# Performance work log

Measured on AMD Instinct MI355X. Metric: run time of the kernel, lower is better.

## Reference

```python
import jax, jax.numpy as jnp
import numpy as np

N = 50000      # nodes per type
E = 200000     # edges per relation
H, D = 4, 64   # heads, per-head dim
C = H * D      # hidden = hc_graph * heads = 256
L = 3          # num_hops (HGTConv layers)
HC_LIN, HC_TASK = 256, 128
OUT_DIMS = (3, 3, 3, 5, 1, 1, 8)  # ptr_l1/l2/l3, leaf_category, signed, floating, size


def setup_inputs() -> dict:
    key = jax.random.key(0)
    ks = jax.random.split(key, 24)
    f = lambda k, s: jax.random.normal(k, s, dtype=jnp.float32) * 0.05
    ri = lambda k: jax.random.randint(k, (E,), 0, N, dtype=jnp.int32)
    return {
        "xe": f(ks[0], (N, C)),
        "xs": f(ks[1], (N, C)),
        "ee_src": ri(ks[2]), "ee_dst": ri(ks[3]),
        "es_src": ri(ks[4]), "es_dst": ri(ks[5]),
        "se_src": ri(ks[6]), "se_dst": ri(ks[7]),
        # per-layer, per-node-type projections (2 node types)
        "Wk": f(ks[8], (L, 2, C, C)),
        "Wq": f(ks[9], (L, 2, C, C)),
        "Wv": f(ks[10], (L, 2, C, C)),
        "Wa": f(ks[11], (L, 2, C, C)),
        "skip": jnp.ones((L, 2), dtype=jnp.float32),
        # per-layer, per-relation attention/message transforms (3 relations)
        "Arel": f(ks[12], (L, 3, H, D, D)),
        "Mrel": f(ks[13], (L, 3, H, D, D)),
        "mu": jnp.ones((L, 3, H), dtype=jnp.float32),
        # shared linear stack + 7 task heads (final out padded to 8, sliced per head)
        "Wsh": f(ks[14], (2, HC_LIN, HC_LIN)),
        "bsh": jnp.zeros((2, HC_LIN), dtype=jnp.float32),
        "Wt1": f(ks[15], (7, HC_LIN, HC_TASK)),
        "bt1": jnp.zeros((7, HC_TASK), dtype=jnp.float32),
        "Wt2": f(ks[16], (7, HC_TASK, 8)),
        "bt2": jnp.zeros((7, 8), dtype=jnp.float32),
    }


def _seg_softmax(scores, seg, n):
    m = jax.ops.segment_max(scores, seg, num_segments=n)
    e = jnp.exp(scores - m[seg])
    s = jax.ops.segment_sum(e, seg, num_segments=n)
    return e / (s[seg] + 1e-16)


def _hgt_forward(xe, xs, ee_src, ee_dst, es_src, es_dst, se_src, se_dst,
                 Wk, Wq, Wv, Wa, skip, Arel, Mrel, mu, Wsh, bsh, Wt1, bt1, Wt2, bt2):
    inv_sqrt_d = 1.0 / jnp.sqrt(jnp.float32(D))

    def rel(k_src, v_src, q_dst, src, dst, A, M, m):
        kt = jnp.einsum('ehd,hdf->ehf', k_src[src], A)          # [E,H,D]
        score = (q_dst[dst] * kt).sum(-1) * (m * inv_sqrt_d)    # [E,H]
        msg = jnp.einsum('ehd,hdf->ehf', v_src[src], M)         # [E,H,D]
        return score, msg

    for l in range(L):
        ke = (xe @ Wk[l, 0]).reshape(N, H, D)
        qe = (xe @ Wq[l, 0]).reshape(N, H, D)
        ve = (xe @ Wv[l, 0]).reshape(N, H, D)
        ks_ = (xs @ Wk[l, 1]).reshape(N, H, D)
        qs = (xs @ Wq[l, 1]).reshape(N, H, D)
        vs = (xs @ Wv[l, 1]).reshape(N, H, D)

        s0, m0 = rel(ke, ve, qe, ee_src, ee_dst, Arel[l, 0], Mrel[l, 0], mu[l, 0])  # expr->expr
        s1, m1 = rel(ke, ve, qs, es_src, es_dst, Arel[l, 1], Mrel[l, 1], mu[l, 1])  # expr->stmt
        s2, m2 = rel(ks_, vs, qe, se_src, se_dst, Arel[l, 2], Mrel[l, 2], mu[l, 2])  # stmt->expr

        # destination 'expr': softmax over all incoming edges (rel0 + rel2)
        sc_e = jnp.concatenate([s0, s2], axis=0)
        ms_e = jnp.concatenate([m0, m2], axis=0)
        dst_e = jnp.concatenate([ee_dst, se_dst], axis=0)
        a_e = _seg_softmax(sc_e, dst_e, N)
        agg_e = jax.ops.segment_sum(a_e[..., None] * ms_e, dst_e, num_segments=N).reshape(N, C)

        # destination 'stmt': only rel1
        a_s = _seg_softmax(s1, es_dst, N)
        agg_s = jax.ops.segment_sum(a_s[..., None] * m1, es_dst, num_segments=N).reshape(N, C)

        be = jax.nn.sigmoid(skip[l, 0])
        bs = jax.nn.sigmoid(skip[l, 1])
        xe = be * (jax.nn.gelu(agg_e, approximate=False) @ Wa[l, 0]) + (1.0 - be) * xe
        xs = bs * (jax.nn.gelu(agg_s, approximate=False) @ Wa[l, 1]) + (1.0 - bs) * xs

    # shared linear stack on 'expr' nodes
    h = xe
    for i in range(Wsh.shape[0]):
        h = jax.nn.relu(h @ Wsh[i] + bsh[i])

    # 7 task heads: hidden layer + final (padded to 8 outputs, sliced per head)
    t = jax.nn.relu(jnp.einsum('nc,kct->knt', h, Wt1) + bt1[:, None, :])  # [7,N,HC_TASK]
    o = jnp.einsum('knt,kto->kno', t, Wt2) + bt2[:, None, :]              # [7,N,8]
    outs = [o[i, :, :d] for i, d in enumerate(OUT_DIMS)]
    return jnp.concatenate(outs, axis=-1)  # [N, 24]


def reference(xe, xs, ee_src, ee_dst, es_src, es_dst, se_src, se_dst,
              Wk, Wq, Wv, Wa, skip, Arel, Mrel, mu, Wsh, bsh, Wt1, bt1, Wt2, bt2):
    return _hgt_forward(xe, xs, ee_src, ee_dst, es_src, es_dst, se_src, se_dst,
                        Wk, Wq, Wv, Wa, skip, Arel, Mrel, mu, Wsh, bsh, Wt1, bt1, Wt2, bt2)
```

## Files before the change

### kernel.cpp

```cpp
#include <hip/hip_runtime.h>
#include <hip/hip_fp16.h>
#include <cmath>


#define CDIM 256
#define AR_R (256 * 256)

using f16x8 = __attribute__((ext_vector_type(8))) _Float16;
using f16x4 = __attribute__((ext_vector_type(4))) _Float16;
using f32x4 = __attribute__((ext_vector_type(4))) float;

__device__ __forceinline__ float gelu_f(float x) {
    return 0.5f * x * (1.0f + erff(x * 0.70710678118654752f));
}
__device__ __forceinline__ float dot4(const f16x4 a, const f16x4 b) {
    return (float)a[0] * (float)b[0] + (float)a[1] * (float)b[1] +
           (float)a[2] * (float)b[2] + (float)a[3] * (float)b[3];
}

__global__ __launch_bounds__(256) void zero_k(int* __restrict__ p, size_t n) {
    size_t i = (size_t)blockIdx.x * blockDim.x + threadIdx.x;
    const size_t stride = (size_t)gridDim.x * blockDim.x;
    for (; i < n; i += stride) p[i] = 0;
}

__global__ __launch_bounds__(256) void cvt_k(const float* __restrict__ in,
                                             _Float16* __restrict__ out,
                                             size_t n4) {
    size_t i = (size_t)blockIdx.x * blockDim.x + threadIdx.x;
    const size_t stride = (size_t)gridDim.x * blockDim.x;
    for (; i < n4; i += stride) {
        const float4 v = ((const float4*)in)[i];
        f16x4 o;
        o[0] = (_Float16)v.x; o[1] = (_Float16)v.y;
        o[2] = (_Float16)v.z; o[3] = (_Float16)v.w;
        ((f16x4*)out)[i] = o;
    }
}

__device__ __forceinline__ void cvtT_dev(const float* __restrict__ W,
                                         _Float16* __restrict__ dst) {
    const int o = blockIdx.x, c = threadIdx.x;
    dst[(size_t)o * 256 + c] = (_Float16)W[(size_t)c * 256 + o];
}

__device__ __forceinline__ void foldT_dev(const float* __restrict__ Wbase,
                                          const float* __restrict__ T,
                                          _Float16* __restrict__ dst) {
    __shared__ float row[256];
    const int c = blockIdx.x, t = threadIdx.x;
    row[t] = Wbase[(size_t)c * 256 + t];
    __syncthreads();
    const int h = t >> 6, f = t & 63;
    const float* Th = T + h * 4096;
    float acc = 0.f;
#pragma unroll 8
    for (int d = 0; d < 64; ++d) acc += row[h * 64 + d] * Th[d * 64 + f];
    dst[(size_t)t * 256 + c] = (_Float16)acc;
}

__global__ __launch_bounds__(256) void prep_layer_k(
    const float* __restrict__ Wk, const float* __restrict__ Wq,
    const float* __restrict__ Wv, const float* __restrict__ Wa,
    const float* __restrict__ Arel, const float* __restrict__ Mrel, int l,
    _Float16* __restrict__ arena) {
    const size_t CC = 65536, HDD = 16384;
    _Float16* L = arena + (size_t)l * 10 * AR_R;
    const float* Wk0 = Wk + (l * 2 + 0) * CC;
    const float* Wk1 = Wk + (l * 2 + 1) * CC;
    const float* Wv0 = Wv + (l * 2 + 0) * CC;
    const float* Wv1 = Wv + (l * 2 + 1) * CC;
    switch (blockIdx.y) {
        case 0: cvtT_dev(Wq + (l * 2 + 0) * CC, L); break;
        case 1: foldT_dev(Wk0, Arel + (l * 3 + 0) * HDD, L + 1 * AR_R); break;
        case 2: foldT_dev(Wk0, Arel + (l * 3 + 1) * HDD, L + 2 * AR_R); break;
        case 3: cvtT_dev(Wq + (l * 2 + 1) * CC, L + 3 * AR_R); break;
        case 4: foldT_dev(Wk1, Arel + (l * 3 + 2) * HDD, L + 4 * AR_R); break;
        case 5: foldT_dev(Wv0, Mrel + (l * 3 + 0) * HDD, L + 5 * AR_R); break;
        case 6: foldT_dev(Wv0, Mrel + (l * 3 + 1) * HDD, L + 6 * AR_R); break;
        case 7: foldT_dev(Wv1, Mrel + (l * 3 + 2) * HDD, L + 7 * AR_R); break;
        case 8: cvtT_dev(Wa + (l * 2 + 0) * CC, L + 8 * AR_R); break;
        case 9: cvtT_dev(Wa + (l * 2 + 1) * CC, L + 9 * AR_R); break;
    }
}

__global__ __launch_bounds__(256) void prep_stack_k(const float* __restrict__ Wsh,
                                                    _Float16* __restrict__ SA) {
    cvtT_dev(Wsh + (size_t)blockIdx.y * 65536, SA + (size_t)blockIdx.y * AR_R);
}

__global__ __launch_bounds__(256) void prep_heads_k(const float* __restrict__ Wt1,
                                                    _Float16* __restrict__ HA) {
    const int o = blockIdx.x, k = blockIdx.y, c = threadIdx.x;
    HA[(size_t)(k * 128 + o) * 256 + c] =
        (_Float16)Wt1[(size_t)k * 256 * 128 + (size_t)c * 128 + o];
}

template <int EPI, bool SPLIT>
__device__ __forceinline__ void gemm_body(
    const _Float16* __restrict__ A, const _Float16* __restrict__ Bt,
    _Float16* __restrict__ C, int M, int Nc, int bn, size_t bufStride,
    const float* __restrict__ bias, const float* __restrict__ skipv,
    _Float16 (*As)[40], _Float16 (*Bs)[40]) {
    const int tid = threadIdx.x;
    const int bm = blockIdx.x * 128;
    const int wave = tid >> 6, lane = tid & 63;
    const int wm = (wave >> 1) * 64, wn = (wave & 1) * 64;
    const int l15 = lane & 15, g = lane >> 4;
    const int srow = tid >> 2, soff = (tid & 3) * 8;

    f32x4 acc[4][4] = {};

    for (int k0 = 0; k0 < 256; k0 += 32) {
        __syncthreads();
#pragma unroll
        for (int p = 0; p < 2; ++p) {
            const int r = p * 64 + srow;
            int gr = bm + r; if (gr >= M) gr = M - 1;
            *(f16x8*)&As[r][soff] =
                *(const f16x8*)&A[(size_t)gr * 256 + k0 + soff];
            *(f16x8*)&Bs[r][soff] =
                *(const f16x8*)&Bt[(size_t)(bn + r) * 256 + k0 + soff];
        }
        __syncthreads();
        f16x8 af[4], bf[4];
#pragma unroll
        for (int i = 0; i < 4; ++i) {
            af[i] = *(const f16x8*)&As[wm + i * 16 + l15][g * 8];
            bf[i] = *(const f16x8*)&Bs[wn + i * 16 + l15][g * 8];
        }
#pragma unroll
        for (int mi = 0; mi < 4; ++mi)
#pragma unroll
            for (int ni = 0; ni < 4; ++ni)
                acc[mi][ni] = __builtin_amdgcn_mfma_f32_16x16x32_f16(
                    af[mi], bf[ni], acc[mi][ni], 0, 0, 0);
    }

    float be = 0.f, ombe = 0.f;
    if (EPI == 1) {
        const float s = skipv[0];
        be = 1.0f / (1.0f + expf(-s));
        ombe = 1.0f - be;
    }
#pragma unroll
    for (int mi = 0; mi < 4; ++mi) {
#pragma unroll
        for (int r = 0; r < 4; ++r) {
            const int row = bm + wm + mi * 16 + g * 4 + r;
            if (row >= M) continue;
#pragma unroll
            for (int ni = 0; ni < 4; ++ni) {
                const int colg = bn + wn + ni * 16 + l15;
                float v = acc[mi][ni][r];
                size_t idx;
                if (SPLIT)
                    idx = (size_t)(colg >> 8) * bufStride + (size_t)row * 256 +
                          (colg & 255);
                else
                    idx = (size_t)row * Nc + colg;
                if (EPI == 1) v = be * v + ombe * (float)C[idx];
                if (EPI == 2) v = fmaxf(v + bias[colg], 0.f);
                C[idx] = (_Float16)v;
            }
        }
    }
}

template <int EPI, bool SPLIT>
__global__ __launch_bounds__(256) void gemm_h(
    const _Float16* __restrict__ A, const _Float16* __restrict__ Bt,
    _Float16* __restrict__ C, int M, int Nc, size_t bufStride,
    const float* __restrict__ bias, const float* __restrict__ skipv) {
    __shared__ _Float16 As[128][40];
    __shared__ _Float16 Bs[128][40];
    gemm_body<EPI, SPLIT>(A, Bt, C, M, Nc, blockIdx.y * 128, bufStride, bias,
                          skipv, As, Bs);
}

__global__ __launch_bounds__(256) void update2_k(
    const _Float16* __restrict__ aggE, const _Float16* __restrict__ aggS,
    const _Float16* __restrict__ WaT0, const _Float16* __restrict__ WaT1,
    _Float16* __restrict__ xeH, _Float16* __restrict__ xsH,
    const float* __restrict__ skipb, int M) {
    __shared__ _Float16 As[128][40];
    __shared__ _Float16 Bs[128][40];
    const int sel = blockIdx.y >> 1;
    const int bn = (blockIdx.y & 1) * 128;
    if (sel == 0)
        gemm_body<1, false>(aggE, WaT0, xeH, M, 256, bn, 0, nullptr, skipb, As, Bs);
    else
        gemm_body<1, false>(aggS, WaT1, xsH, M, 256, bn, 0, nullptr, skipb + 1, As, Bs);
}

__global__ __launch_bounds__(256) void hist3_k(const int* __restrict__ d0,
                                               const int* __restrict__ d1,
                                               const int* __restrict__ d2,
                                               int* __restrict__ cnt, int N,
                                               int E) {
    const int i = blockIdx.x * 256 + threadIdx.x;
    if (i >= E) return;
    const int r = blockIdx.y;
    const int* d = r == 0 ? d0 : r == 1 ? d1 : d2;
    atomicAdd(&cnt[(size_t)r * N + d[i]], 1);
}

__global__ __launch_bounds__(1024) void scan3_k(const int* __restrict__ cnt,
                                                int* __restrict__ rp, int N) {
    __shared__ int sums[1024];
    const int r = blockIdx.y;
    const int* c = cnt + (size_t)r * N;
    int* o = rp + (size_t)r * (N + 1);
    const int tid = threadIdx.x;
    const int chunk = (N + 1023) / 1024;
    const int lo = min(tid * chunk, N), hi = min(lo + chunk, N);
    int s = 0;
    for (int i = lo; i < hi; ++i) s += c[i];
    sums[tid] = s;
    __syncthreads();
    for (int off = 1; off < 1024; off <<= 1) {
        const int v = (tid >= off) ? sums[tid - off] : 0;
        __syncthreads();
        sums[tid] += v;
        __syncthreads();
    }
    int run = (tid == 0) ? 0 : sums[tid - 1];
    for (int i = lo; i < hi; ++i) { o[i] = run; run += c[i]; }
    if (tid == 1023) o[N] = run;
}

__global__ __launch_bounds__(256) void scatter3_k(
    const int* __restrict__ d0, const int* __restrict__ d1,
    const int* __restrict__ d2, const int* __restrict__ s0_,
    const int* __restrict__ s1_, const int* __restrict__ s2_,
    const int* __restrict__ rp, int* __restrict__ fill,
    int* __restrict__ colsrc, int N, int E) {
    const int i = blockIdx.x * 256 + threadIdx.x;
    if (i >= E) return;
    const int r = blockIdx.y;
    const int* d = r == 0 ? d0 : r == 1 ? d1 : d2;
    const int* s = r == 0 ? s0_ : r == 1 ? s1_ : s2_;
    const int dd = d[i];
    const int p = rp[(size_t)r * (N + 1) + dd] + atomicAdd(&fill[(size_t)r * N + dd], 1);
    colsrc[(size_t)r * E + p] = s[i];
}

__device__ __forceinline__ void score_rel(
    const f16x4 qv, const _Float16* __restrict__ kA,
    const int* __restrict__ cs, int beg, int end, float scale,
    float* __restrict__ sc, int lane, int h, float& m, float& den) {
    int i = beg;
    for (; i + 1 < end; i += 2) {
        const int sA = cs[i], sB = cs[i + 1];
        const f16x4 k0 = *(const f16x4*)&kA[(size_t)sA * 256 + lane * 4];
        const f16x4 k1 = *(const f16x4*)&kA[(size_t)sB * 256 + lane * 4];
        float p0 = dot4(qv, k0), p1 = dot4(qv, k1);
        p0 += __shfl_xor(p0, 1); p1 += __shfl_xor(p1, 1);
        p0 += __shfl_xor(p0, 2); p1 += __shfl_xor(p1, 2);
        p0 += __shfl_xor(p0, 4); p1 += __shfl_xor(p1, 4);
        p0 += __shfl_xor(p0, 8); p1 += __shfl_xor(p1, 8);
        const float v0 = p0 * scale, v1 = p1 * scale;
        if ((lane & 15) == 0) {
            sc[(size_t)i * 4 + h] = v0;
            sc[(size_t)(i + 1) * 4 + h] = v1;
        }
        const float nm = fmaxf(m, fmaxf(v0, v1));
        den = den * expf(m - nm) + expf(v0 - nm) + expf(v1 - nm);
        m = nm;
    }
    if (i < end) {
        const int sA = cs[i];
        const f16x4 k0 = *(const f16x4*)&kA[(size_t)sA * 256 + lane * 4];
        float p0 = dot4(qv, k0);
        p0 += __shfl_xor(p0, 1); p0 += __shfl_xor(p0, 2);
        p0 += __shfl_xor(p0, 4); p0 += __shfl_xor(p0, 8);
        const float v0 = p0 * scale;
        if ((lane & 15) == 0) sc[(size_t)i * 4 + h] = v0;
        const float nm = fmaxf(m, v0);
        den = den * expf(m - nm) + expf(v0 - nm);
        m = nm;
    }
}

__global__ __launch_bounds__(256) void score3_k(
    const _Float16* __restrict__ qe, const _Float16* __restrict__ kA0,
    const _Float16* __restrict__ kA1, const _Float16* __restrict__ qs,
    const _Float16* __restrict__ kA2, const int* __restrict__ rp,
    const int* __restrict__ colsrc, const float* __restrict__ muL,
    float* __restrict__ sc, float* __restrict__ mx_e,
    float* __restrict__ den_e, float* __restrict__ mx_s,
    float* __restrict__ den_s, int N, int E) {
    const int wid = (blockIdx.x * blockDim.x + threadIdx.x) >> 6;
    if (wid >= N) return;
    const int lane = threadIdx.x & 63;
    const int h = lane >> 4;
    const size_t E4 = (size_t)E * 4;
    float m = -1e30f, den = 0.f;
    if (blockIdx.y == 0) {
        const f16x4 qv = *(const f16x4*)&qe[(size_t)wid * 256 + lane * 4];
        score_rel(qv, kA0, colsrc, rp[wid], rp[wid + 1],
                  muL[0 * 4 + h] * 0.125f, sc, lane, h, m, den);
        const int* rp2 = rp + 2 * (N + 1);
        score_rel(qv, kA2, colsrc + 2 * (size_t)E, rp2[wid], rp2[wid + 1],
                  muL[2 * 4 + h] * 0.125f, sc + 2 * E4, lane, h, m, den);
        if ((lane & 15) == 0) {
            mx_e[(size_t)wid * 4 + h] = m;
            den_e[(size_t)wid * 4 + h] = den;
        }
    } else {
        const f16x4 qv = *(const f16x4*)&qs[(size_t)wid * 256 + lane * 4];
        const int* rp1 = rp + (N + 1);
        score_rel(qv, kA1, colsrc + (size_t)E, rp1[wid], rp1[wid + 1],
                  muL[1 * 4 + h] * 0.125f, sc + E4, lane, h, m, den);
        if ((lane & 15) == 0) {
            mx_s[(size_t)wid * 4 + h] = m;
            den_s[(size_t)wid * 4 + h] = den;
        }
    }
}

__device__ __forceinline__ void agg_rel(const float* __restrict__ sc,
                                        const _Float16* __restrict__ vM,
                                        const int* __restrict__ cs, int beg,
                                        int end, float m, float dinv, int lane,
                                        int h, float4& acc) {
    int i = beg;
    for (; i + 1 < end; i += 2) {
        const int sA = cs[i], sB = cs[i + 1];
        const float w0 = expf(sc[(size_t)i * 4 + h] - m) * dinv;
        const float w1 = expf(sc[(size_t)(i + 1) * 4 + h] - m) * dinv;
        const f16x4 v0 = *(const f16x4*)&vM[(size_t)sA * 256 + lane * 4];
        const f16x4 v1 = *(const f16x4*)&vM[(size_t)sB * 256 + lane * 4];
        acc.x += w0 * (float)v0[0] + w1 * (float)v1[0];
        acc.y += w0 * (float)v0[1] + w1 * (float)v1[1];
        acc.z += w0 * (float)v0[2] + w1 * (float)v1[2];
        acc.w += w0 * (float)v0[3] + w1 * (float)v1[3];
    }
    if (i < end) {
        const int sA = cs[i];
        const float w0 = expf(sc[(size_t)i * 4 + h] - m) * dinv;
        const f16x4 v0 = *(const f16x4*)&vM[(size_t)sA * 256 + lane * 4];
        acc.x += w0 * (float)v0[0]; acc.y += w0 * (float)v0[1];
        acc.z += w0 * (float)v0[2]; acc.w += w0 * (float)v0[3];
    }
}

__global__ __launch_bounds__(256) void agg3_k(
    const float* __restrict__ sc, const _Float16* __restrict__ vM0,
    const _Float16* __restrict__ vM1, const _Float16* __restrict__ vM2,
    const int* __restrict__ rp, const int* __restrict__ colsrc,
    const float* __restrict__ mx_e, const float* __restrict__ den_e,
    const float* __restrict__ mx_s, const float* __restrict__ den_s,
    _Float16* __restrict__ outE, _Float16* __restrict__ outS, int N, int E) {
    const int wid = (blockIdx.x * blockDim.x + threadIdx.x) >> 6;
    if (wid >= N) return;
    const int lane = threadIdx.x & 63;
    const int h = lane >> 4;
    const size_t E4 = (size_t)E * 4;
    float4 acc = make_float4(0.f, 0.f, 0.f, 0.f);
    if (blockIdx.y == 0) {
        const float m = mx_e[(size_t)wid * 4 + h];
        const float dinv = 1.0f / (den_e[(size_t)wid * 4 + h] + 1e-16f);
        agg_rel(sc, vM0, colsrc, rp[wid], rp[wid + 1], m, dinv, lane, h, acc);
        const int* rp2 = rp + 2 * (N + 1);
        agg_rel(sc + 2 * E4, vM2, colsrc + 2 * (size_t)E, rp2[wid],
                rp2[wid + 1], m, dinv, lane, h, acc);
        f16x4 o;
        o[0] = (_Float16)gelu_f(acc.x); o[1] = (_Float16)gelu_f(acc.y);
        o[2] = (_Float16)gelu_f(acc.z); o[3] = (_Float16)gelu_f(acc.w);
        *(f16x4*)&outE[(size_t)wid * 256 + lane * 4] = o;
    } else {
        const float m = mx_s[(size_t)wid * 4 + h];
        const float dinv = 1.0f / (den_s[(size_t)wid * 4 + h] + 1e-16f);
        const int* rp1 = rp + (N + 1);
        agg_rel(sc + E4, vM1, colsrc + (size_t)E, rp1[wid], rp1[wid + 1], m,
                dinv, lane, h, acc);
        f16x4 o;
        o[0] = (_Float16)gelu_f(acc.x); o[1] = (_Float16)gelu_f(acc.y);
        o[2] = (_Float16)gelu_f(acc.z); o[3] = (_Float16)gelu_f(acc.w);
        *(f16x4*)&outS[(size_t)wid * 256 + lane * 4] = o;
    }
}

__global__ __launch_bounds__(256) void head2_k(const _Float16* __restrict__ t,
                                               const float* __restrict__ Wt2,
                                               const float* __restrict__ bt2,
                                               float* __restrict__ out, int M) {
    const int k = blockIdx.y;
    __shared__ float Ws[128 * 8];
    __shared__ float bs[8];
    const int tid = threadIdx.x;
    const float* W2 = Wt2 + (size_t)k * 1024;
    for (int i = tid; i < 1024; i += 256) Ws[i] = W2[i];
    if (tid < 8) bs[tid] = bt2[k * 8 + tid];
    __syncthreads();
    const int OFFA[7] = {0, 3, 6, 9, 14, 15, 16};
    const int DIMSA[7] = {3, 3, 3, 5, 1, 1, 8};
    const int nl = tid >> 3, o = tid & 7;
    const int n = blockIdx.x * 32 + nl;
    if (n >= M) return;
    const _Float16* tr = &t[(size_t)n * 896 + k * 128];
    float acc = bs[o];
#pragma unroll 8
    for (int d = 0; d < 128; ++d) acc += (float)tr[d] * Ws[d * 8 + o];
    if (o < DIMSA[k]) out[(size_t)n * 24 + OFFA[k] + o] = acc;
}


extern "C" void kernel_launch(void* const* d_in, const int* in_sizes, int n_in,
                              void* d_out, int out_size, void* d_ws,
                              size_t ws_size, hipStream_t stream) {
    const float* xe_in = (const float*)d_in[0];
    const float* xs_in = (const float*)d_in[1];
    const int* ee_src = (const int*)d_in[2];
    const int* ee_dst = (const int*)d_in[3];
    const int* es_src = (const int*)d_in[4];
    const int* es_dst = (const int*)d_in[5];
    const int* se_src = (const int*)d_in[6];
    const int* se_dst = (const int*)d_in[7];
    const float* Wk = (const float*)d_in[8];
    const float* Wq = (const float*)d_in[9];
    const float* Wv = (const float*)d_in[10];
    const float* Wa = (const float*)d_in[11];
    const float* skip = (const float*)d_in[12];
    const float* Arel = (const float*)d_in[13];
    const float* Mrel = (const float*)d_in[14];
    const float* mu = (const float*)d_in[15];
    const float* Wsh = (const float*)d_in[16];
    const float* bsh = (const float*)d_in[17];
    const float* Wt1 = (const float*)d_in[18];
    const float* bt1 = (const float*)d_in[19];
    const float* Wt2 = (const float*)d_in[20];
    const float* bt2 = (const float*)d_in[21];
    float* out = (float*)d_out;

    const int N = in_sizes[0] / CDIM;
    const int E = in_sizes[2];
    const size_t NC = (size_t)N * CDIM;
    const size_t E4 = (size_t)E * 4;
    const size_t N4 = (size_t)N * 4;

    const size_t halfs = 7 * NC + 32 * (size_t)AR_R + 7 * 32768;
    const size_t floats = 3 * E4 + 4 * N4;
    const size_t ints = 3 * (size_t)(N + 1) + 3 * (size_t)E + 3 * (size_t)N;
    const size_t need = halfs * 2 + floats * 4 + ints * 4;
    if (ws_size < need) return;

    _Float16* xeH = (_Float16*)d_ws;
    _Float16* xsH = xeH + NC;
    _Float16* Hb = xsH + NC;
    _Float16* H1 = Hb;
    _Float16* H2 = Hb + NC;
    _Float16* H3 = Hb + 2 * NC;
    _Float16* H4 = Hb + 3 * NC;
    _Float16* H5 = Hb + 4 * NC;
    _Float16* arena = Hb + 5 * NC;
    _Float16* SA = arena + (size_t)30 * AR_R;
    _Float16* HA = SA + (size_t)2 * AR_R;
    float* sc = (float*)(HA + (size_t)7 * 32768);
    float* mx_e = sc + 3 * E4;
    float* den_e = mx_e + N4;
    float* mx_s = den_e + N4;
    float* den_s = mx_s + N4;
    int* rp = (int*)(den_s + N4);
    int* colsrc = rp + 3 * (size_t)(N + 1);
    int* cnt = colsrc + 3 * (size_t)E;

    const int gx = (N + 127) / 128;
    const dim3 e3((E + 255) / 256, 3);
    const int wave_blocks = (N + 3) / 4;
    const int zc_blocks = (3 * N + 255) / 256;

    zero_k<<<zc_blocks, 256, 0, stream>>>(cnt, 3 * (size_t)N);
    hist3_k<<<e3, 256, 0, stream>>>(ee_dst, es_dst, se_dst, cnt, N, E);
    scan3_k<<<dim3(1, 3), 1024, 0, stream>>>(cnt, rp, N);
    zero_k<<<zc_blocks, 256, 0, stream>>>(cnt, 3 * (size_t)N);
    scatter3_k<<<e3, 256, 0, stream>>>(ee_dst, es_dst, se_dst, ee_src, es_src,
                                       se_src, rp, cnt, colsrc, N, E);

    for (int l = 0; l < 3; ++l)
        prep_layer_k<<<dim3(256, 10), 256, 0, stream>>>(Wk, Wq, Wv, Wa, Arel,
                                                        Mrel, l, arena);
    prep_stack_k<<<dim3(256, 2), 256, 0, stream>>>(Wsh, SA);
    prep_heads_k<<<dim3(128, 7), 256, 0, stream>>>(Wt1, HA);

    cvt_k<<<1024, 256, 0, stream>>>(xe_in, xeH, NC / 4);
    cvt_k<<<1024, 256, 0, stream>>>(xs_in, xsH, NC / 4);

    for (int l = 0; l < 3; ++l) {
        _Float16* L = arena + (size_t)l * 10 * AR_R;
        gemm_h<0, true><<<dim3(gx, 6), 256, 0, stream>>>(
            xeH, L, H1, N, 768, NC, nullptr, nullptr);
        gemm_h<0, true><<<dim3(gx, 4), 256, 0, stream>>>(
            xsH, L + 3 * AR_R, H4, N, 512, NC, nullptr, nullptr);
        score3_k<<<dim3(wave_blocks, 2), 256, 0, stream>>>(
            H1, H2, H3, H4, H5, rp, colsrc, mu + l * 12, sc, mx_e, den_e, mx_s,
            den_s, N, E);
        gemm_h<0, true><<<dim3(gx, 4), 256, 0, stream>>>(
            xeH, L + 5 * AR_R, H2, N, 512, NC, nullptr, nullptr);
        gemm_h<0, false><<<dim3(gx, 2), 256, 0, stream>>>(
            xsH, L + 7 * AR_R, H5, N, 256, 0, nullptr, nullptr);
        agg3_k<<<dim3(wave_blocks, 2), 256, 0, stream>>>(
            sc, H2, H3, H5, rp, colsrc, mx_e, den_e, mx_s, den_s, H1, H4, N, E);
        update2_k<<<dim3(gx, 4), 256, 0, stream>>>(
            H1, H4, L + 8 * AR_R, L + 9 * AR_R, xeH, xsH, skip + l * 2, N);
    }

    gemm_h<2, false><<<dim3(gx, 2), 256, 0, stream>>>(xeH, SA, H5, N, 256, 0,
                                                      bsh, nullptr);
    gemm_h<2, false><<<dim3(gx, 2), 256, 0, stream>>>(H5, SA + AR_R, xsH, N,
                                                      256, 0, bsh + 256, nullptr);
    gemm_h<2, false><<<dim3(gx, 7), 256, 0, stream>>>(xsH, HA, Hb, N, 896, 0,
                                                      bt1, nullptr);
    head2_k<<<dim3((N + 31) / 32, 7), 256, 0, stream>>>(Hb, Wt2, bt2, out, N);
}
```

Before: 1.282 ms.

## Use XOR-swizzled 64-wide K tiles, fdot2 scoring, and move softmax denominator to aggregation

The shared GEMM body now stages 64-wide K tiles in an XOR-swizzled LDS layout instead of padded 32-wide tiles. This halves the number of barrier-separated iterations and is meant to avoid bank conflicts. The score kernel now uses the fdot2 builtin for its half-precision dot products and tracks only the running max, dropping the online-softmax exp work. The aggregation kernel recomputes the softmax denominator from the stored scores in a separate pass, which adds extra score reads and exps there but removes the den buffers.

```diff
diff --git a/kernel.cpp b/kernel.cpp
--- a/kernel.cpp
+++ b/kernel.cpp
@@ -8,14 +8,23 @@
 
 using f16x8 = __attribute__((ext_vector_type(8))) _Float16;
 using f16x4 = __attribute__((ext_vector_type(4))) _Float16;
+using f16x2 = __attribute__((ext_vector_type(2))) _Float16;
 using f32x4 = __attribute__((ext_vector_type(4))) float;
 
 __device__ __forceinline__ float gelu_f(float x) {
     return 0.5f * x * (1.0f + erff(x * 0.70710678118654752f));
 }
-__device__ __forceinline__ float dot4(const f16x4 a, const f16x4 b) {
+
+__device__ __forceinline__ float dot4f(const f16x4 a, const f16x4 b) {
+#if __has_builtin(__builtin_amdgcn_fdot2)
+    f16x2 al = {a[0], a[1]}, ah = {a[2], a[3]};
+    f16x2 bl = {b[0], b[1]}, bh = {b[2], b[3]};
+    float r = __builtin_amdgcn_fdot2(al, bl, 0.0f, false);
+    return __builtin_amdgcn_fdot2(ah, bh, r, false);
+#else
     return (float)a[0] * (float)b[0] + (float)a[1] * (float)b[1] +
            (float)a[2] * (float)b[2] + (float)a[3] * (float)b[3];
+#endif
 }
 
 __global__ __launch_bounds__(256) void zero_k(int* __restrict__ p, size_t n) {
@@ -101,40 +110,51 @@
     const _Float16* __restrict__ A, const _Float16* __restrict__ Bt,
     _Float16* __restrict__ C, int M, int Nc, int bn, size_t bufStride,
     const float* __restrict__ bias, const float* __restrict__ skipv,
-    _Float16 (*As)[40], _Float16 (*Bs)[40]) {
+    _Float16* As, _Float16* Bs) {
     const int tid = threadIdx.x;
     const int bm = blockIdx.x * 128;
     const int wave = tid >> 6, lane = tid & 63;
     const int wm = (wave >> 1) * 64, wn = (wave & 1) * 64;
     const int l15 = lane & 15, g = lane >> 4;
-    const int srow = tid >> 2, soff = (tid & 3) * 8;
+    const int srow = tid >> 3;
+    const int sbyte = (tid & 7) * 16;
 
     f32x4 acc[4][4] = {};
 
-    for (int k0 = 0; k0 < 256; k0 += 32) {
+    for (int k0 = 0; k0 < 256; k0 += 64) {
         __syncthreads();
 #pragma unroll
-        for (int p = 0; p < 2; ++p) {
-            const int r = p * 64 + srow;
+        for (int p = 0; p < 4; ++p) {
+            const int r = p * 32 + srow;
             int gr = bm + r; if (gr >= M) gr = M - 1;
-            *(f16x8*)&As[r][soff] =
-                *(const f16x8*)&A[(size_t)gr * 256 + k0 + soff];
-            *(f16x8*)&Bs[r][soff] =
-                *(const f16x8*)&Bt[(size_t)(bn + r) * 256 + k0 + soff];
+            const f16x8 av = *(const f16x8*)((const char*)A +
+                                             ((size_t)gr * 256 + k0) * 2 + sbyte);
+            const f16x8 bv = *(const f16x8*)((const char*)Bt +
+                                             ((size_t)(bn + r) * 256 + k0) * 2 + sbyte);
+            const int wb = sbyte ^ ((r & 7) << 4);
+            *(f16x8*)((char*)As + r * 128 + wb) = av;
+            *(f16x8*)((char*)Bs + r * 128 + wb) = bv;
         }
         __syncthreads();
-        f16x8 af[4], bf[4];
-#pragma unroll
-        for (int i = 0; i < 4; ++i) {
-            af[i] = *(const f16x8*)&As[wm + i * 16 + l15][g * 8];
-            bf[i] = *(const f16x8*)&Bs[wn + i * 16 + l15][g * 8];
+#pragma unroll
+        for (int sub = 0; sub < 2; ++sub) {
+            f16x8 af[4], bf[4];
+#pragma unroll
+            for (int i = 0; i < 4; ++i) {
+                const int ra = wm + i * 16 + l15;
+                const int rb = wn + i * 16 + l15;
+                const int ka = (sub * 64 + g * 16) ^ ((ra & 7) << 4);
+                const int kb = (sub * 64 + g * 16) ^ ((rb & 7) << 4);
+                af[i] = *(const f16x8*)((const char*)As + ra * 128 + ka);
+                bf[i] = *(const f16x8*)((const char*)Bs + rb * 128 + kb);
+            }
+#pragma unroll
+            for (int mi = 0; mi < 4; ++mi)
+#pragma unroll
+                for (int ni = 0; ni < 4; ++ni)
+                    acc[mi][ni] = __builtin_amdgcn_mfma_f32_16x16x32_f16(
+                        af[mi], bf[ni], acc[mi][ni], 0, 0, 0);
         }
-#pragma unroll
-        for (int mi = 0; mi < 4; ++mi)
-#pragma unroll
-            for (int ni = 0; ni < 4; ++ni)
-                acc[mi][ni] = __builtin_amdgcn_mfma_f32_16x16x32_f16(
-                    af[mi], bf[ni], acc[mi][ni], 0, 0, 0);
     }
 
     float be = 0.f, ombe = 0.f;
@@ -172,8 +192,8 @@
     const _Float16* __restrict__ A, const _Float16* __restrict__ Bt,
     _Float16* __restrict__ C, int M, int Nc, size_t bufStride,
     const float* __restrict__ bias, const float* __restrict__ skipv) {
-    __shared__ _Float16 As[128][40];
-    __shared__ _Float16 Bs[128][40];
+    __shared__ _Float16 As[128 * 64];
+    __shared__ _Float16 Bs[128 * 64];
     gemm_body<EPI, SPLIT>(A, Bt, C, M, Nc, blockIdx.y * 128, bufStride, bias,
                           skipv, As, Bs);
 }
@@ -183,8 +203,8 @@
     const _Float16* __restrict__ WaT0, const _Float16* __restrict__ WaT1,
     _Float16* __restrict__ xeH, _Float16* __restrict__ xsH,
     const float* __restrict__ skipb, int M) {
-    __shared__ _Float16 As[128][40];
-    __shared__ _Float16 Bs[128][40];
+    __shared__ _Float16 As[128 * 64];
+    __shared__ _Float16 Bs[128 * 64];
     const int sel = blockIdx.y >> 1;
     const int bn = (blockIdx.y & 1) * 128;
     if (sel == 0)
@@ -248,13 +268,13 @@
 __device__ __forceinline__ void score_rel(
     const f16x4 qv, const _Float16* __restrict__ kA,
     const int* __restrict__ cs, int beg, int end, float scale,
-    float* __restrict__ sc, int lane, int h, float& m, float& den) {
+    float* __restrict__ sc, int lane, int h, float& m) {
     int i = beg;
     for (; i + 1 < end; i += 2) {
         const int sA = cs[i], sB = cs[i + 1];
         const f16x4 k0 = *(const f16x4*)&kA[(size_t)sA * 256 + lane * 4];
         const f16x4 k1 = *(const f16x4*)&kA[(size_t)sB * 256 + lane * 4];
-        float p0 = dot4(qv, k0), p1 = dot4(qv, k1);
+        float p0 = dot4f(qv, k0), p1 = dot4f(qv, k1);
         p0 += __shfl_xor(p0, 1); p1 += __shfl_xor(p1, 1);
         p0 += __shfl_xor(p0, 2); p1 += __shfl_xor(p1, 2);
         p0 += __shfl_xor(p0, 4); p1 += __shfl_xor(p1, 4);
@@ -264,21 +284,17 @@
             sc[(size_t)i * 4 + h] = v0;
             sc[(size_t)(i + 1) * 4 + h] = v1;
         }
-        const float nm = fmaxf(m, fmaxf(v0, v1));
-        den = den * expf(m - nm) + expf(v0 - nm) + expf(v1 - nm);
-        m = nm;
+        m = fmaxf(m, fmaxf(v0, v1));
     }
     if (i < end) {
         const int sA = cs[i];
         const f16x4 k0 = *(const f16x4*)&kA[(size_t)sA * 256 + lane * 4];
-        float p0 = dot4(qv, k0);
+        float p0 = dot4f(qv, k0);
         p0 += __shfl_xor(p0, 1); p0 += __shfl_xor(p0, 2);
         p0 += __shfl_xor(p0, 4); p0 += __shfl_xor(p0, 8);
         const float v0 = p0 * scale;
         if ((lane & 15) == 0) sc[(size_t)i * 4 + h] = v0;
-        const float nm = fmaxf(m, v0);
-        den = den * expf(m - nm) + expf(v0 - nm);
-        m = nm;
+        m = fmaxf(m, v0);
     }
 }
 
@@ -288,34 +304,27 @@
     const _Float16* __restrict__ kA2, const int* __restrict__ rp,
     const int* __restrict__ colsrc, const float* __restrict__ muL,
     float* __restrict__ sc, float* __restrict__ mx_e,
-    float* __restrict__ den_e, float* __restrict__ mx_s,
-    float* __restrict__ den_s, int N, int E) {
+    float* __restrict__ mx_s, int N, int E) {
     const int wid = (blockIdx.x * blockDim.x + threadIdx.x) >> 6;
     if (wid >= N) return;
     const int lane = threadIdx.x & 63;
     const int h = lane >> 4;
     const size_t E4 = (size_t)E * 4;
-    float m = -1e30f, den = 0.f;
+    float m = -1e30f;
     if (blockIdx.y == 0) {
         const f16x4 qv = *(const f16x4*)&qe[(size_t)wid * 256 + lane * 4];
         score_rel(qv, kA0, colsrc, rp[wid], rp[wid + 1],
-                  muL[0 * 4 + h] * 0.125f, sc, lane, h, m, den);
+                  muL[0 * 4 + h] * 0.125f, sc, lane, h, m);
         const int* rp2 = rp + 2 * (N + 1);
         score_rel(qv, kA2, colsrc + 2 * (size_t)E, rp2[wid], rp2[wid + 1],
-                  muL[2 * 4 + h] * 0.125f, sc + 2 * E4, lane, h, m, den);
-        if ((lane & 15) == 0) {
-            mx_e[(size_t)wid * 4 + h] = m;
-            den_e[(size_t)wid * 4 + h] = den;
-        }
+                  muL[2 * 4 + h] * 0.125f, sc + 2 * E4, lane, h, m);
+        if ((lane & 15) == 0) mx_e[(size_t)wid * 4 + h] = m;
     } else {
         const f16x4 qv = *(const f16x4*)&qs[(size_t)wid * 256 + lane * 4];
         const int* rp1 = rp + (N + 1);
         score_rel(qv, kA1, colsrc + (size_t)E, rp1[wid], rp1[wid + 1],
-                  muL[1 * 4 + h] * 0.125f, sc + E4, lane, h, m, den);
-        if ((lane & 15) == 0) {
-            mx_s[(size_t)wid * 4 + h] = m;
-            den_s[(size_t)wid * 4 + h] = den;
-        }
+                  muL[1 * 4 + h] * 0.125f, sc + E4, lane, h, m);
+        if ((lane & 15) == 0) mx_s[(size_t)wid * 4 + h] = m;
     }
 }
 
@@ -349,32 +358,50 @@
     const float* __restrict__ sc, const _Float16* __restrict__ vM0,
     const _Float16* __restrict__ vM1, const _Float16* __restrict__ vM2,
     const int* __restrict__ rp, const int* __restrict__ colsrc,
-    const float* __restrict__ mx_e, const float* __restrict__ den_e,
-    const float* __restrict__ mx_s, const float* __restrict__ den_s,
+    const float* __restrict__ mx_e, const float* __restrict__ mx_s,
     _Float16* __restrict__ outE, _Float16* __restrict__ outS, int N, int E) {
     const int wid = (blockIdx.x * blockDim.x + threadIdx.x) >> 6;
     if (wid >= N) return;
     const int lane = threadIdx.x & 63;
-    const int h = lane >> 4;
+    const int hHi = lane >> 4, hLo = lane & 3, sl = lane >> 2;
     const size_t E4 = (size_t)E * 4;
     float4 acc = make_float4(0.f, 0.f, 0.f, 0.f);
     if (blockIdx.y == 0) {
-        const float m = mx_e[(size_t)wid * 4 + h];
-        const float dinv = 1.0f / (den_e[(size_t)wid * 4 + h] + 1e-16f);
-        agg_rel(sc, vM0, colsrc, rp[wid], rp[wid + 1], m, dinv, lane, h, acc);
+        const float mLo = mx_e[(size_t)wid * 4 + hLo];
+        const float mHi = mx_e[(size_t)wid * 4 + hHi];
+        const int b0 = rp[wid], e0 = rp[wid + 1];
         const int* rp2 = rp + 2 * (N + 1);
-        agg_rel(sc + 2 * E4, vM2, colsrc + 2 * (size_t)E, rp2[wid],
-                rp2[wid + 1], m, dinv, lane, h, acc);
+        const int b2 = rp2[wid], e2 = rp2[wid + 1];
+        const float* sc2 = sc + 2 * E4;
+        float dl = 0.f;
+        for (int i = b0 + sl; i < e0; i += 16)
+            dl += expf(sc[(size_t)i * 4 + hLo] - mLo);
+        for (int i = b2 + sl; i < e2; i += 16)
+            dl += expf(sc2[(size_t)i * 4 + hLo] - mLo);
+        dl += __shfl_xor(dl, 4); dl += __shfl_xor(dl, 8);
+        dl += __shfl_xor(dl, 16); dl += __shfl_xor(dl, 32);
+        const float dinv = 1.0f / (__shfl(dl, hHi) + 1e-16f);
+        agg_rel(sc, vM0, colsrc, b0, e0, mHi, dinv, lane, hHi, acc);
+        agg_rel(sc2, vM2, colsrc + 2 * (size_t)E, b2, e2, mHi, dinv, lane, hHi,
+                acc);
         f16x4 o;
         o[0] = (_Float16)gelu_f(acc.x); o[1] = (_Float16)gelu_f(acc.y);
         o[2] = (_Float16)gelu_f(acc.z); o[3] = (_Float16)gelu_f(acc.w);
         *(f16x4*)&outE[(size_t)wid * 256 + lane * 4] = o;
     } else {
-        const float m = mx_s[(size_t)wid * 4 + h];
-        const float dinv = 1.0f / (den_s[(size_t)wid * 4 + h] + 1e-16f);
+        const float mLo = mx_s[(size_t)wid * 4 + hLo];
+        const float mHi = mx_s[(size_t)wid * 4 + hHi];
         const int* rp1 = rp + (N + 1);
-        agg_rel(sc + E4, vM1, colsrc + (size_t)E, rp1[wid], rp1[wid + 1], m,
-                dinv, lane, h, acc);
+        const int b1 = rp1[wid], e1 = rp1[wid + 1];
+        const float* sc1 = sc + E4;
+        float dl = 0.f;
+        for (int i = b1 + sl; i < e1; i += 16)
+            dl += expf(sc1[(size_t)i * 4 + hLo] - mLo);
+        dl += __shfl_xor(dl, 4); dl += __shfl_xor(dl, 8);
+        dl += __shfl_xor(dl, 16); dl += __shfl_xor(dl, 32);
+        const float dinv = 1.0f / (__shfl(dl, hHi) + 1e-16f);
+        agg_rel(sc1, vM1, colsrc + (size_t)E, b1, e1, mHi, dinv, lane, hHi,
+                acc);
         f16x4 o;
         o[0] = (_Float16)gelu_f(acc.x); o[1] = (_Float16)gelu_f(acc.y);
         o[2] = (_Float16)gelu_f(acc.z); o[3] = (_Float16)gelu_f(acc.w);
@@ -441,7 +468,7 @@
     const size_t N4 = (size_t)N * 4;
 
     const size_t halfs = 7 * NC + 32 * (size_t)AR_R + 7 * 32768;
-    const size_t floats = 3 * E4 + 4 * N4;
+    const size_t floats = 3 * E4 + 2 * N4;
     const size_t ints = 3 * (size_t)(N + 1) + 3 * (size_t)E + 3 * (size_t)N;
     const size_t need = halfs * 2 + floats * 4 + ints * 4;
     if (ws_size < need) return;
@@ -459,10 +486,8 @@
     _Float16* HA = SA + (size_t)2 * AR_R;
     float* sc = (float*)(HA + (size_t)7 * 32768);
     float* mx_e = sc + 3 * E4;
-    float* den_e = mx_e + N4;
-    float* mx_s = den_e + N4;
-    float* den_s = mx_s + N4;
-    int* rp = (int*)(den_s + N4);
+    float* mx_s = mx_e + N4;
+    int* rp = (int*)(mx_s + N4);
     int* colsrc = rp + 3 * (size_t)(N + 1);
     int* cnt = colsrc + 3 * (size_t)E;
 
@@ -494,14 +519,13 @@
         gemm_h<0, true><<<dim3(gx, 4), 256, 0, stream>>>(
             xsH, L + 3 * AR_R, H4, N, 512, NC, nullptr, nullptr);
         score3_k<<<dim3(wave_blocks, 2), 256, 0, stream>>>(
-            H1, H2, H3, H4, H5, rp, colsrc, mu + l * 12, sc, mx_e, den_e, mx_s,
-            den_s, N, E);
+            H1, H2, H3, H4, H5, rp, colsrc, mu + l * 12, sc, mx_e, mx_s, N, E);
         gemm_h<0, true><<<dim3(gx, 4), 256, 0, stream>>>(
             xeH, L + 5 * AR_R, H2, N, 512, NC, nullptr, nullptr);
         gemm_h<0, false><<<dim3(gx, 2), 256, 0, stream>>>(
             xsH, L + 7 * AR_R, H5, N, 256, 0, nullptr, nullptr);
         agg3_k<<<dim3(wave_blocks, 2), 256, 0, stream>>>(
-            sc, H2, H3, H5, rp, colsrc, mx_e, den_e, mx_s, den_s, H1, H4, N, E);
+            sc, H2, H3, H5, rp, colsrc, mx_e, mx_s, H1, H4, N, E);
         update2_k<<<dim3(gx, 4), 256, 0, stream>>>(
             H1, H4, L + 8 * AR_R, L + 9 * AR_R, xeH, xsH, skip + l * 2, N);
     }
```

Measured after the change: 1.251 ms. 1.02x faster.
